# Performance work log

Measured on AMD Instinct MI355X. Metric: run time of the kernel, lower is better.

Reference implementation:

```python
import jax, jax.numpy as jnp
import numpy as np

N_NODES = 50000


def _degree_norm(src, dst, n):
    # symmetric GCN normalization with self-loops already appended
    deg = jax.ops.segment_sum(jnp.ones(src.shape[0], jnp.float32), dst, num_segments=n)
    dinv = jnp.where(deg > 0, jax.lax.rsqrt(deg), 0.0)
    return dinv[src] * dinv[dst]  # [E_full]


def _gcn_layer(x, W, b, src, dst, norm, n):
    h = x @ W                                  # [N, out]
    msgs = h[src] * norm[:, None]              # gather + scale, [E_full, out]
    out = jax.ops.segment_sum(msgs, dst, num_segments=n)
    return out + b


def setup_inputs() -> dict:
    key = jax.random.key(0)
    k1, k2, k3, k4 = jax.random.split(key, 4)
    n, e, d_in, d_out = N_NODES, 800000, 256, 128
    x = jax.random.normal(k1, (n, d_in), jnp.float32)
    edge_index = jax.random.randint(k2, (2, e), 0, n, dtype=jnp.int64)
    W1 = jax.random.normal(k3, (d_in, 2 * d_out), jnp.float32) / np.sqrt(d_in)
    b1 = jnp.zeros((2 * d_out,), jnp.float32)
    W2 = jax.random.normal(k4, (2 * d_out, d_out), jnp.float32) / np.sqrt(2 * d_out)
    b2 = jnp.zeros((d_out,), jnp.float32)
    return {"x": x, "edge_index": edge_index, "W1": W1, "b1": b1, "W2": W2, "b2": b2}


def reference(x, edge_index, W1, b1, W2, b2):
    n = x.shape[0]
    loops = jnp.arange(n, dtype=edge_index.dtype)
    src = jnp.concatenate([edge_index[0], loops])
    dst = jnp.concatenate([edge_index[1], loops])
    norm = _degree_norm(src, dst, n)
    h = jax.nn.relu(_gcn_layer(x, W1, b1, src, dst, norm, n))
    h = jax.nn.relu(_gcn_layer(h, W2, b2, src, dst, norm, n))
    return h
```

## Files before the change

kernel.cpp:

```cpp
#include <hip/hip_runtime.h>
#include <hip/hip_bf16.h>


typedef __attribute__((ext_vector_type(8))) short bf16x8;
typedef __attribute__((ext_vector_type(8))) unsigned short u16x8;
typedef __attribute__((ext_vector_type(4))) float f32x4;

__device__ inline float bf2f(unsigned short u) {
    return __uint_as_float(((unsigned)u) << 16);
}
__device__ inline unsigned short f2bf(float f) {
    unsigned x = __float_as_uint(f);
    unsigned r = (x + 0x7fffu + ((x >> 16) & 1u)) >> 16;
    return (unsigned short)r;
}

#define NBIN 512

__global__ void degree_kernel(const int* __restrict__ dst, unsigned* __restrict__ deg, int E) {
    int e = blockIdx.x * blockDim.x + threadIdx.x;
    if (e < E) atomicAdd(&deg[dst[e]], 1u);
}

__global__ __launch_bounds__(256) void dinv_hist_kernel(const unsigned* __restrict__ deg,
                                                        float* __restrict__ dinv,
                                                        int* __restrict__ hist, int N) {
    __shared__ int lh[NBIN];
    const int t = threadIdx.x;
#pragma unroll
    for (int i = 0; i < NBIN / 256; i++) lh[t + i * 256] = 0;
    __syncthreads();
    int idx = blockIdx.x * 256 + t;
    if (idx < N) {
        unsigned d = deg[idx];
        dinv[idx] = rsqrtf((float)(d + 1u));
        int b = (int)d; if (b > NBIN - 1) b = NBIN - 1;
        atomicAdd(&lh[NBIN - 1 - b], 1);
    }
    __syncthreads();
#pragma unroll
    for (int i = 0; i < NBIN / 256; i++) {
        int v = lh[t + i * 256];
        if (v) atomicAdd(&hist[t + i * 256], v);
    }
}

__global__ __launch_bounds__(256) void place_fused_kernel(
    const unsigned* __restrict__ deg,
    const int* __restrict__ hist,
    int* __restrict__ binres,
    int* __restrict__ perm,
    int* __restrict__ rowptr, int* __restrict__ cursor,
    unsigned short* __restrict__ col, int N) {
    __shared__ int lh[NBIN];
    __shared__ int base[NBIN];
    __shared__ int binstartL[NBIN];
    __shared__ int edgebaseL[NBIN];
    const int t = threadIdx.x;
#pragma unroll
    for (int i = 0; i < NBIN / 256; i++) lh[t + i * 256] = 0;
    __syncthreads();
    if (t < 64) {
        int cn = 0, ce = 0;
        for (int b = 0; b < NBIN; b += 64) {
            int i = b + t;
            int cnt = hist[i];
            int d = NBIN - 1 - i;
            int d8 = (d + 7) & ~7;
            int en = cnt * d8;
            int xn = cnt, xe = en;
#pragma unroll
            for (int off = 1; off < 64; off <<= 1) {
                int yn = __shfl_up(xn, off, 64);
                int ye = __shfl_up(xe, off, 64);
                if (t >= off) { xn += yn; xe += ye; }
            }
            binstartL[i] = cn + xn - cnt;
            edgebaseL[i] = ce + xe - en;
            cn += __shfl(xn, 63, 64);
            ce += __shfl(xe, 63, 64);
        }
    }
    int idx = blockIdx.x * 256 + t;
    int bin = 0, lrank = 0;
    if (idx < N) {
        int b = (int)deg[idx]; if (b > NBIN - 1) b = NBIN - 1;
        bin = NBIN - 1 - b;
        lrank = atomicAdd(&lh[bin], 1);
    }
    __syncthreads();
    if (blockIdx.x == 0 && t == 0) rowptr[N] = edgebaseL[NBIN - 1];
#pragma unroll
    for (int i = 0; i < NBIN / 256; i++) {
        int v = lh[t + i * 256];
        if (v) base[t + i * 256] = binstartL[t + i * 256] +
                                   atomicAdd(&binres[t + i * 256], v);
    }
    __syncthreads();
    if (idx < N) {
        int pos = base[bin] + lrank;
        int d = NBIN - 1 - bin;
        int d8 = (d + 7) & ~7;
        int rp = edgebaseL[bin] + (pos - binstartL[bin]) * d8;
        perm[pos] = idx;
        rowptr[pos] = rp;
        cursor[idx] = rp;
        for (int k = d; k < d8; k++) col[rp + k] = (unsigned short)N;
    }
}

__global__ __launch_bounds__(256) void fill_kernel(const int* __restrict__ src,
                                                   const int* __restrict__ dst,
                                                   int* __restrict__ cursor,
                                                   unsigned short* __restrict__ col, int E) {
    int e = blockIdx.x * blockDim.x + threadIdx.x;
    if (e < E) {
        int d = dst[e];
        int pos = atomicAdd(&cursor[d], 1);
        col[pos] = (unsigned short)src[e];
    }
}

__global__ __launch_bounds__(256) void convwt_pad_kernel(
    const float* __restrict__ W1, const float* __restrict__ W2,
    unsigned short* __restrict__ w1t, unsigned short* __restrict__ w2t,
    unsigned short* __restrict__ h1b, unsigned short* __restrict__ h2b,
    int DIN, int H, int DOUT, int Np1) {
    int id = blockIdx.x * 256 + threadIdx.x;
    int n1 = DIN * H;
    int n2 = H * DOUT;
    if (id < n1) {
        int k = id / H, n = id % H;
        w1t[(long)n * DIN + k] = f2bf(W1[id]);
    } else if (id < n1 + n2) {
        int q = id - n1;
        int k = q / DOUT, n = q % DOUT;
        w2t[(long)n * H + k] = f2bf(W2[q]);
    } else if (id < n1 + n2 + 384) {
        int q = id - n1 - n2;
        if (q < 256) {
            int c = q >> 5, f = q & 31;
            h1b[((size_t)c * Np1 + (Np1 - 1)) * 32 + f] = 0;
        } else {
            int q2 = q - 256;
            int c = q2 >> 5, f = q2 & 31;
            h2b[((size_t)c * Np1 + (Np1 - 1)) * 32 + f] = 0;
        }
    }
}

#define GBM 128
#define GBN 128
#define GBK 64
__global__ __launch_bounds__(256) void gemm_x_bf16(const float* __restrict__ X,
                                                   const float* __restrict__ dinv,
                                                   const unsigned short* __restrict__ BT,
                                                   unsigned short* __restrict__ C,
                                                   int M, int K, int ldm) {
    __shared__ __align__(16) unsigned short As[GBM * GBK];
    __shared__ __align__(16) unsigned short Bs[2][GBN * GBK];
    const int t = threadIdx.x;
    const int lane = t & 63;
    const int w = t >> 6;
    const int row0 = blockIdx.x * GBM;
    const int rb = (w >> 1) * 64;
    const int cb = (w & 1) * 64;

    f32x4 acc[2][4][4] = {};

    for (int kb = 0; kb < K; kb += GBK) {
#pragma unroll
        for (int i = 0; i < 4; i++) {
            int p = i * 256 + t;
            int row = p >> 3;
            int slot = p & 7;
            int chunk = slot ^ (row & 7);
            int grow = row0 + row;
            if (grow >= M) grow = M - 1;
            const float* sp = X + (size_t)grow * K + kb + chunk * 8;
            f32x4 v0 = *(const f32x4*)sp;
            f32x4 v1 = *(const f32x4*)(sp + 4);
            float ds = dinv[grow];
            u16x8 o;
#pragma unroll
            for (int j = 0; j < 4; j++) { o[j] = f2bf(v0[j] * ds); o[j + 4] = f2bf(v1[j] * ds); }
            *(u16x8*)&As[p * 8] = o;
        }
#pragma unroll
        for (int ct = 0; ct < 2; ct++)
#pragma unroll
            for (int i = 0; i < 4; i++) {
                int p = i * 256 + t;
                int row = p >> 3;
                int slot = p & 7;
                int chunk = slot ^ (row & 7);
                const unsigned short* src = BT + (size_t)(ct * GBN + row) * K + kb + chunk * 8;
                __builtin_amdgcn_global_load_lds(
                    (const __attribute__((address_space(1))) void*)src,
                    (__attribute__((address_space(3))) void*)&Bs[ct][p * 8], 16, 0, 0);
            }
        asm volatile("s_waitcnt vmcnt(0)" ::: "memory");
        __syncthreads();

#pragma unroll
        for (int ks = 0; ks < 2; ks++) {
            int kq = ks * 4 + (lane >> 4);
            int rsel = lane & 15;
            bf16x8 af[4];
#pragma unroll
            for (int mt = 0; mt < 4; mt++) {
                int m = rb + mt * 16 + rsel;
                int slot = kq ^ (m & 7);
                af[mt] = *(const bf16x8*)&As[m * GBK + slot * 8];
            }
#pragma unroll
            for (int ct = 0; ct < 2; ct++) {
                bf16x8 bfr[4];
#pragma unroll
                for (int nt = 0; nt < 4; nt++) {
                    int n = cb + nt * 16 + rsel;
                    int slot = kq ^ (n & 7);
                    bfr[nt] = *(const bf16x8*)&Bs[ct][n * GBK + slot * 8];
                }
#pragma unroll
                for (int mt = 0; mt < 4; mt++)
#pragma unroll
                    for (int nt = 0; nt < 4; nt++)
                        acc[ct][mt][nt] = __builtin_amdgcn_mfma_f32_16x16x32_bf16(
                            af[mt], bfr[nt], acc[ct][mt][nt], 0, 0, 0);
            }
        }
        __syncthreads();
    }

#pragma unroll
    for (int ct = 0; ct < 2; ct++)
#pragma unroll
        for (int mt = 0; mt < 4; mt++)
#pragma unroll
            for (int nt = 0; nt < 4; nt++) {
                int gcol = ct * GBN + cb + nt * 16 + (lane & 15);
                int c = gcol >> 5;
                int fo = gcol & 31;
                int grow0 = row0 + rb + mt * 16 + 4 * (lane >> 4);
#pragma unroll
                for (int r = 0; r < 4; r++) {
                    int g = grow0 + r;
                    if (g < M)
                        C[((size_t)c * ldm + g) * 32 + fo] = f2bf(acc[ct][mt][nt][r]);
                }
            }
}

template <int CH>
__global__ __launch_bounds__(256) void gemm_bf16(const unsigned short* __restrict__ A,
                                                 const unsigned short* __restrict__ BT,
                                                 unsigned short* __restrict__ C,
                                                 int M, int Nc, int K, int ldm) {
    __shared__ __align__(16) unsigned short As[GBM * GBK];
    __shared__ __align__(16) unsigned short Bs[GBN * GBK];
    const int t = threadIdx.x;
    const int lane = t & 63;
    const int w = t >> 6;
    const int row0 = blockIdx.x * GBM;
    const int col0 = blockIdx.y * GBN;
    const int rb = (w >> 1) * 64;
    const int cb = (w & 1) * 64;

    f32x4 acc[4][4] = {};

    for (int kb = 0; kb < K; kb += GBK) {
#pragma unroll
        for (int i = 0; i < 4; i++) {
            int p = i * 256 + t;
            int row = p >> 3;
            int slot = p & 7;
            int chunk = slot ^ (row & 7);
            int grow = row0 + row;
            if (grow >= M) grow = M - 1;
            const unsigned short* src = A + (size_t)grow * K + kb + chunk * 8;
            __builtin_amdgcn_global_load_lds(
                (const __attribute__((address_space(1))) void*)src,
                (__attribute__((address_space(3))) void*)&As[p * 8], 16, 0, 0);
        }
#pragma unroll
        for (int i = 0; i < 4; i++) {
            int p = i * 256 + t;
            int row = p >> 3;
            int slot = p & 7;
            int chunk = slot ^ (row & 7);
            const unsigned short* src = BT + (size_t)(col0 + row) * K + kb + chunk * 8;
            __builtin_amdgcn_global_load_lds(
                (const __attribute__((address_space(1))) void*)src,
                (__attribute__((address_space(3))) void*)&Bs[p * 8], 16, 0, 0);
        }
        asm volatile("s_waitcnt vmcnt(0)" ::: "memory");
        __syncthreads();

#pragma unroll
        for (int ks = 0; ks < 2; ks++) {
            int kq = ks * 4 + (lane >> 4);
            int rsel = lane & 15;
            bf16x8 af[4], bfr[4];
#pragma unroll
            for (int mt = 0; mt < 4; mt++) {
                int m = rb + mt * 16 + rsel;
                int slot = kq ^ (m & 7);
                af[mt] = *(const bf16x8*)&As[m * GBK + slot * 8];
            }
#pragma unroll
            for (int nt = 0; nt < 4; nt++) {
                int n = cb + nt * 16 + rsel;
                int slot = kq ^ (n & 7);
                bfr[nt] = *(const bf16x8*)&Bs[n * GBK + slot * 8];
            }
#pragma unroll
            for (int mt = 0; mt < 4; mt++)
#pragma unroll
                for (int nt = 0; nt < 4; nt++)
                    acc[mt][nt] = __builtin_amdgcn_mfma_f32_16x16x32_bf16(
                        af[mt], bfr[nt], acc[mt][nt], 0, 0, 0);
        }
        __syncthreads();
    }

#pragma unroll
    for (int mt = 0; mt < 4; mt++) {
#pragma unroll
        for (int nt = 0; nt < 4; nt++) {
            int gcol = col0 + cb + nt * 16 + (lane & 15);
            int c = gcol / CH;
            int fo = gcol % CH;
            int grow0 = row0 + rb + mt * 16 + 4 * (lane >> 4);
#pragma unroll
            for (int r = 0; r < 4; r++) {
                int g = grow0 + r;
                if (g < M)
                    C[((size_t)c * ldm + g) * CH + fo] = f2bf(acc[mt][nt][r]);
            }
        }
    }
}

template <int CH, int NCH, bool OUT_BF16>
__global__ __launch_bounds__(512) void gather_cm_kernel(
    const unsigned short* __restrict__ h_cm,
    const int* __restrict__ rowptr,
    const unsigned short* __restrict__ col,
    const int* __restrict__ perm,
    const float* __restrict__ dinv,
    const float* __restrict__ bias,
    void* __restrict__ out,
    int Nn, int F) {
    constexpr int LF = CH / 8;
    constexpr int NS = 64 / LF;
    constexpr int NPB = NS * 8;
    const int chunk = blockIdx.x % NCH;
    const int g = blockIdx.x / NCH;
    const int w = threadIdx.x >> 6;
    const int lane = threadIdx.x & 63;
    const int fl = lane & (LF - 1);
    const int ns = lane / LF;
    const int idx = g * NPB + w * NS + ns;
    const bool valid = idx < Nn;
    const int cidx = valid ? idx : Nn - 1;
    const int node = perm[cidx];

    const unsigned short* hc = h_cm + (size_t)chunk * (Nn + 1) * CH;
    const int beg = rowptr[cidx];
    const int nit = (rowptr[cidx + 1] - beg) >> 3;
    const float ddst = dinv[node];
    const int fo = fl * 8;

    float a0[8] = {}, a1[8] = {};
    const unsigned short* cp = col + beg;
    u16x8 cv = *(const u16x8*)cp;
    for (int it = 0; it < nit; ++it) {
        int s0 = cv[0], s1 = cv[1], s2 = cv[2], s3 = cv[3];
        int s4 = cv[4], s5 = cv[5], s6 = cv[6], s7 = cv[7];
        u16x8 u0 = *(const u16x8*)(hc + s0 * CH + fo);
        u16x8 u1 = *(const u16x8*)(hc + s1 * CH + fo);
        u16x8 u2 = *(const u16x8*)(hc + s2 * CH + fo);
        u16x8 u3 = *(const u16x8*)(hc + s3 * CH + fo);
        u16x8 u4 = *(const u16x8*)(hc + s4 * CH + fo);
        u16x8 u5 = *(const u16x8*)(hc + s5 * CH + fo);
        u16x8 u6 = *(const u16x8*)(hc + s6 * CH + fo);
        u16x8 u7 = *(const u16x8*)(hc + s7 * CH + fo);
        cp += 8;
        cv = *(const u16x8*)cp;
#pragma unroll
        for (int j = 0; j < 8; j++) {
            a0[j] += (bf2f(u0[j]) + bf2f(u1[j])) + (bf2f(u2[j]) + bf2f(u3[j]));
            a1[j] += (bf2f(u4[j]) + bf2f(u5[j])) + (bf2f(u6[j]) + bf2f(u7[j]));
        }
    }

    if (valid) {
        u16x8 us = *(const u16x8*)(hc + node * CH + fo);
        const int f0g = chunk * CH + fo;
        f32x4 bv0 = *(const f32x4*)(bias + f0g);
        f32x4 bv1 = *(const f32x4*)(bias + f0g + 4);
        float v[8];
#pragma unroll
        for (int j = 0; j < 8; j++) {
            float b = (j < 4) ? bv0[j] : bv1[j - 4];
            float s = (a0[j] + a1[j]) + bf2f(us[j]);
            v[j] = fmaxf(fmaf(s, ddst, b), 0.f);
        }
        if (OUT_BF16) {
            u16x8 o;
#pragma unroll
            for (int j = 0; j < 8; j++) o[j] = f2bf(v[j] * ddst);
            *(u16x8*)((unsigned short*)out + (size_t)node * F + f0g) = o;
        } else {
            f32x4 o0, o1;
#pragma unroll
            for (int j = 0; j < 4; j++) { o0[j] = v[j]; o1[j] = v[j + 4]; }
            float* op = (float*)out + (size_t)node * F + f0g;
            *(f32x4*)op = o0;
            *(f32x4*)(op + 4) = o1;
        }
    }
}

extern "C" void kernel_launch(void* const* d_in, const int* in_sizes, int n_in,
                              void* d_out, int out_size, void* d_ws, size_t ws_size,
                              hipStream_t stream) {
    const float* x  = (const float*)d_in[0];
    const int* ei   = (const int*)d_in[1];
    const float* W1 = (const float*)d_in[2];
    const float* b1 = (const float*)d_in[3];
    const float* W2 = (const float*)d_in[4];
    const float* b2 = (const float*)d_in[5];

    const int DIN = 256;
    const int N = in_sizes[0] / DIN;
    const int E = in_sizes[1] / 2;
    const int H = in_sizes[3];
    const int DOUT = in_sizes[5];

    const int* src = ei;
    const int* dst = ei + E;

    char* ws = (char*)d_ws;
    unsigned* deg = (unsigned*)ws;                   ws += (size_t)N * 4;
    int* hist     = (int*)ws;                        ws += NBIN * 4;
    int* binres   = (int*)ws;                        ws += NBIN * 4;
    float* dinv   = (float*)ws;                      ws += (size_t)N * 4;
    int* rowptr   = (int*)ws;                        ws += (size_t)(N + 4) * 4;
    int* perm     = (int*)ws;                        ws += (size_t)N * 4;
    int* cursor   = (int*)ws;                        ws += (size_t)N * 4;
    unsigned short* col = (unsigned short*)ws;       ws += (size_t)(E + 8 * N + 64) * 2;
    unsigned short* w1t = (unsigned short*)ws;       ws += (size_t)DIN * H * 2;
    unsigned short* w2t = (unsigned short*)ws;       ws += (size_t)H * DOUT * 2;
    unsigned short* h1b = (unsigned short*)ws;       ws += (size_t)(N + 1) * H * 2 + 1024;
    unsigned short* y1b = (unsigned short*)ws;       ws += (size_t)N * H * 2;
    unsigned short* h2b = (unsigned short*)ws;       ws += (size_t)(N + 1) * DOUT * 2 + 1024;
    float* outp = (float*)d_out;

    hipMemsetAsync(deg, 0, (size_t)N * 4 + (size_t)2 * NBIN * 4, stream);
    degree_kernel<<<(E + 255) / 256, 256, 0, stream>>>(dst, deg, E);
    dinv_hist_kernel<<<(N + 255) / 256, 256, 0, stream>>>(deg, dinv, hist, N);
    place_fused_kernel<<<(N + 255) / 256, 256, 0, stream>>>(
        deg, hist, binres, perm, rowptr, cursor, col, N);
    fill_kernel<<<(E + 255) / 256, 256, 0, stream>>>(src, dst, cursor, col, E);

    {
        int tot = DIN * H + H * DOUT + 384;
        convwt_pad_kernel<<<(tot + 255) / 256, 256, 0, stream>>>(
            W1, W2, w1t, w2t, h1b, h2b, DIN, H, DOUT, N + 1);
    }

    {
        dim3 grid((N + GBM - 1) / GBM, 1);
        gemm_x_bf16<<<grid, 256, 0, stream>>>(x, dinv, w1t, h1b, N, DIN, N + 1);
    }
    {
        constexpr int NPB1 = (64 / (32 / 8)) * 8;
        gather_cm_kernel<32, 8, true><<<8 * ((N + NPB1 - 1) / NPB1), 512, 0, stream>>>(
            h1b, rowptr, col, perm, dinv, b1, y1b, N, H);
    }

    {
        dim3 grid((N + GBM - 1) / GBM, DOUT / GBN);
        gemm_bf16<32><<<grid, 256, 0, stream>>>(y1b, w2t, h2b, N, DOUT, H, N + 1);
    }
    {
        constexpr int NPB2 = (64 / (32 / 8)) * 8;
        gather_cm_kernel<32, 4, false><<<4 * ((N + NPB2 - 1) / NPB2), 512, 0, stream>>>(
            h2b, rowptr, col, perm, dinv, b2, outp, N, DOUT);
    }
}
```

Measured before the change: 315.4 us.

## Fuse graph-build preprocessing into one cooperative kernel with grid syncs

```diff
diff --git a/kernel.cpp b/kernel.cpp
--- a/kernel.cpp
+++ b/kernel.cpp
@@ -1,10 +1,13 @@
 #include <hip/hip_runtime.h>
 #include <hip/hip_bf16.h>
+#include <hip/hip_cooperative_groups.h>
 
 
 typedef __attribute__((ext_vector_type(8))) short bf16x8;
 typedef __attribute__((ext_vector_type(8))) unsigned short u16x8;
 typedef __attribute__((ext_vector_type(4))) float f32x4;
+
+namespace cg = cooperative_groups;
 
 __device__ inline float bf2f(unsigned short u) {
     return __uint_as_float(((unsigned)u) << 16);
@@ -17,49 +20,79 @@
 
 #define NBIN 512
 
-__global__ void degree_kernel(const int* __restrict__ dst, unsigned* __restrict__ deg, int E) {
-    int e = blockIdx.x * blockDim.x + threadIdx.x;
-    if (e < E) atomicAdd(&deg[dst[e]], 1u);
-}
-
-__global__ __launch_bounds__(256) void dinv_hist_kernel(const unsigned* __restrict__ deg,
-                                                        float* __restrict__ dinv,
-                                                        int* __restrict__ hist, int N) {
+__global__ __launch_bounds__(256) void build_kernel(
+    const int* __restrict__ src, const int* __restrict__ dst,
+    const float* __restrict__ W1, const float* __restrict__ W2,
+    unsigned* __restrict__ deg, int* __restrict__ hist, int* __restrict__ binres,
+    float* __restrict__ dinv, int* __restrict__ perm,
+    int* __restrict__ rowptr, int* __restrict__ cursor,
+    unsigned short* __restrict__ col,
+    unsigned short* __restrict__ w1t, unsigned short* __restrict__ w2t,
+    unsigned short* __restrict__ h1b, unsigned short* __restrict__ h2b,
+    int N, int E, int DIN, int H, int DOUT, int Np1) {
+    cg::grid_group grid = cg::this_grid();
+    const int t = threadIdx.x;
+    const int gid = blockIdx.x * 256 + t;
+    const int gsz = gridDim.x * 256;
+
     __shared__ int lh[NBIN];
-    const int t = threadIdx.x;
-#pragma unroll
-    for (int i = 0; i < NBIN / 256; i++) lh[t + i * 256] = 0;
-    __syncthreads();
-    int idx = blockIdx.x * 256 + t;
-    if (idx < N) {
-        unsigned d = deg[idx];
-        dinv[idx] = rsqrtf((float)(d + 1u));
-        int b = (int)d; if (b > NBIN - 1) b = NBIN - 1;
-        atomicAdd(&lh[NBIN - 1 - b], 1);
-    }
-    __syncthreads();
-#pragma unroll
-    for (int i = 0; i < NBIN / 256; i++) {
-        int v = lh[t + i * 256];
-        if (v) atomicAdd(&hist[t + i * 256], v);
-    }
-}
-
-__global__ __launch_bounds__(256) void place_fused_kernel(
-    const unsigned* __restrict__ deg,
-    const int* __restrict__ hist,
-    int* __restrict__ binres,
-    int* __restrict__ perm,
-    int* __restrict__ rowptr, int* __restrict__ cursor,
-    unsigned short* __restrict__ col, int N) {
-    __shared__ int lh[NBIN];
-    __shared__ int base[NBIN];
+    __shared__ int base_s[NBIN];
     __shared__ int binstartL[NBIN];
     __shared__ int edgebaseL[NBIN];
-    const int t = threadIdx.x;
-#pragma unroll
-    for (int i = 0; i < NBIN / 256; i++) lh[t + i * 256] = 0;
-    __syncthreads();
+
+    for (int i = gid; i < N; i += gsz) deg[i] = 0u;
+    for (int i = gid; i < 2 * NBIN; i += gsz) {
+        if (i < NBIN) hist[i] = 0; else binres[i - NBIN] = 0;
+    }
+    {
+        int n1 = DIN * H, n2 = H * DOUT;
+        for (int id = gid; id < n1 + n2 + 384; id += gsz) {
+            if (id < n1) {
+                int k = id / H, n = id % H;
+                w1t[(long)n * DIN + k] = f2bf(W1[id]);
+            } else if (id < n1 + n2) {
+                int q = id - n1;
+                int k = q / DOUT, n = q % DOUT;
+                w2t[(long)n * H + k] = f2bf(W2[q]);
+            } else {
+                int q = id - n1 - n2;
+                if (q < 256) {
+                    int c = q >> 5, f = q & 31;
+                    h1b[((size_t)c * Np1 + (Np1 - 1)) * 32 + f] = 0;
+                } else {
+                    int q2 = q - 256;
+                    int c = q2 >> 5, f = q2 & 31;
+                    h2b[((size_t)c * Np1 + (Np1 - 1)) * 32 + f] = 0;
+                }
+            }
+        }
+    }
+    grid.sync();
+
+    for (int e = gid; e < E; e += gsz) atomicAdd(&deg[dst[e]], 1u);
+    grid.sync();
+
+    {
+        int i0 = blockIdx.x * 256;
+        if (i0 < N) {
+            for (int i = t; i < NBIN; i += 256) lh[i] = 0;
+            __syncthreads();
+            int idx = i0 + t;
+            if (idx < N) {
+                unsigned d = deg[idx];
+                dinv[idx] = rsqrtf((float)(d + 1u));
+                int b = (int)d; if (b > NBIN - 1) b = NBIN - 1;
+                atomicAdd(&lh[NBIN - 1 - b], 1);
+            }
+            __syncthreads();
+            for (int i = t; i < NBIN; i += 256) {
+                int v = lh[i];
+                if (v) atomicAdd(&hist[i], v);
+            }
+        }
+    }
+    grid.sync();
+
     if (t < 64) {
         int cn = 0, ce = 0;
         for (int b = 0; b < NBIN; b += 64) {
@@ -81,71 +114,44 @@
             ce += __shfl(xe, 63, 64);
         }
     }
-    int idx = blockIdx.x * 256 + t;
-    int bin = 0, lrank = 0;
-    if (idx < N) {
-        int b = (int)deg[idx]; if (b > NBIN - 1) b = NBIN - 1;
-        bin = NBIN - 1 - b;
-        lrank = atomicAdd(&lh[bin], 1);
-    }
     __syncthreads();
     if (blockIdx.x == 0 && t == 0) rowptr[N] = edgebaseL[NBIN - 1];
-#pragma unroll
-    for (int i = 0; i < NBIN / 256; i++) {
-        int v = lh[t + i * 256];
-        if (v) base[t + i * 256] = binstartL[t + i * 256] +
-                                   atomicAdd(&binres[t + i * 256], v);
-    }
-    __syncthreads();
-    if (idx < N) {
-        int pos = base[bin] + lrank;
-        int d = NBIN - 1 - bin;
-        int d8 = (d + 7) & ~7;
-        int rp = edgebaseL[bin] + (pos - binstartL[bin]) * d8;
-        perm[pos] = idx;
-        rowptr[pos] = rp;
-        cursor[idx] = rp;
-        for (int k = d; k < d8; k++) col[rp + k] = (unsigned short)N;
-    }
-}
-
-__global__ __launch_bounds__(256) void fill_kernel(const int* __restrict__ src,
-                                                   const int* __restrict__ dst,
-                                                   int* __restrict__ cursor,
-                                                   unsigned short* __restrict__ col, int E) {
-    int e = blockIdx.x * blockDim.x + threadIdx.x;
-    if (e < E) {
+    {
+        int i0 = blockIdx.x * 256;
+        if (i0 < N) {
+            for (int i = t; i < NBIN; i += 256) lh[i] = 0;
+            __syncthreads();
+            int idx = i0 + t;
+            int bin = 0, lrank = 0;
+            if (idx < N) {
+                int b = (int)deg[idx]; if (b > NBIN - 1) b = NBIN - 1;
+                bin = NBIN - 1 - b;
+                lrank = atomicAdd(&lh[bin], 1);
+            }
+            __syncthreads();
+            for (int i = t; i < NBIN; i += 256) {
+                int v = lh[i];
+                if (v) base_s[i] = binstartL[i] + atomicAdd(&binres[i], v);
+            }
+            __syncthreads();
+            if (idx < N) {
+                int pos = base_s[bin] + lrank;
+                int d = NBIN - 1 - bin;
+                int d8 = (d + 7) & ~7;
+                int rp = edgebaseL[bin] + (pos - binstartL[bin]) * d8;
+                perm[pos] = idx;
+                rowptr[pos] = rp;
+                cursor[idx] = rp;
+                for (int k = d; k < d8; k++) col[rp + k] = (unsigned short)N;
+            }
+        }
+    }
+    grid.sync();
+
+    for (int e = gid; e < E; e += gsz) {
         int d = dst[e];
         int pos = atomicAdd(&cursor[d], 1);
         col[pos] = (unsigned short)src[e];
-    }
-}
-
-__global__ __launch_bounds__(256) void convwt_pad_kernel(
-    const float* __restrict__ W1, const float* __restrict__ W2,
-    unsigned short* __restrict__ w1t, unsigned short* __restrict__ w2t,
-    unsigned short* __restrict__ h1b, unsigned short* __restrict__ h2b,
-    int DIN, int H, int DOUT, int Np1) {
-    int id = blockIdx.x * 256 + threadIdx.x;
-    int n1 = DIN * H;
-    int n2 = H * DOUT;
-    if (id < n1) {
-        int k = id / H, n = id % H;
-        w1t[(long)n * DIN + k] = f2bf(W1[id]);
-    } else if (id < n1 + n2) {
-        int q = id - n1;
-        int k = q / DOUT, n = q % DOUT;
-        w2t[(long)n * H + k] = f2bf(W2[q]);
-    } else if (id < n1 + n2 + 384) {
-        int q = id - n1 - n2;
-        if (q < 256) {
-            int c = q >> 5, f = q & 31;
-            h1b[((size_t)c * Np1 + (Np1 - 1)) * 32 + f] = 0;
-        } else {
-            int q2 = q - 256;
-            int c = q2 >> 5, f = q2 & 31;
-            h2b[((size_t)c * Np1 + (Np1 - 1)) * 32 + f] = 0;
-        }
     }
 }
 
@@ -458,17 +464,19 @@
     unsigned short* h2b = (unsigned short*)ws;       ws += (size_t)(N + 1) * DOUT * 2 + 1024;
     float* outp = (float*)d_out;
 
-    hipMemsetAsync(deg, 0, (size_t)N * 4 + (size_t)2 * NBIN * 4, stream);
-    degree_kernel<<<(E + 255) / 256, 256, 0, stream>>>(dst, deg, E);
-    dinv_hist_kernel<<<(N + 255) / 256, 256, 0, stream>>>(deg, dinv, hist, N);
-    place_fused_kernel<<<(N + 255) / 256, 256, 0, stream>>>(
-        deg, hist, binres, perm, rowptr, cursor, col, N);
-    fill_kernel<<<(E + 255) / 256, 256, 0, stream>>>(src, dst, cursor, col, E);
-
-    {
-        int tot = DIN * H + H * DOUT + 384;
-        convwt_pad_kernel<<<(tot + 255) / 256, 256, 0, stream>>>(
-            W1, W2, w1t, w2t, h1b, h2b, DIN, H, DOUT, N + 1);
+    {
+        int Nl = N, El = E, DINl = DIN, Hl = H, DOUTl = DOUT, Np1 = N + 1;
+        const int* srcl = src; const int* dstl = dst;
+        const float* W1l = W1; const float* W2l = W2;
+        void* args[] = {
+            (void*)&srcl, (void*)&dstl, (void*)&W1l, (void*)&W2l,
+            (void*)&deg, (void*)&hist, (void*)&binres, (void*)&dinv,
+            (void*)&perm, (void*)&rowptr, (void*)&cursor, (void*)&col,
+            (void*)&w1t, (void*)&w2t, (void*)&h1b, (void*)&h2b,
+            (void*)&Nl, (void*)&El, (void*)&DINl, (void*)&Hl, (void*)&DOUTl, (void*)&Np1
+        };
+        hipLaunchCooperativeKernel((const void*)build_kernel,
+                                   dim3(512), dim3(256), args, 0, stream);
     }
 
     {
```

Result: slower. 553.6 us (+75.5%).
